# Performance work log

Hardware: AMD Instinct MI355X
Metric: run time of the kernel (lower is better)

## Reference

```python
import jax, jax.numpy as jnp
import numpy as np

B = 4096        # batch_size
D = 256         # feature_dim
N = 9000000     # dataset size (state buffer length)
G = 100         # num_groups
ALPHA = 0.5     # alpha_weight
GAMMA = 0.8
RHO = 8.0
LAM = 1.0       # lambada
ETA_P = 0.01
EPS = 1e-14
CLIP = 5.0


def setup_inputs() -> dict:
    key = jax.random.key(0)
    k = jax.random.split(key, 6)
    zis = jax.random.normal(k[0], (B, D), jnp.float32)
    zjs = jax.random.normal(k[1], (B, D), jnp.float32)
    # per-sample learned temperatures, small positive values
    taus_I = 0.01 + 0.2 * jax.random.uniform(k[2], (N,), jnp.float32)
    taus_T = 0.01 + 0.2 * jax.random.uniform(k[3], (N,), jnp.float32)
    group_info_I = jax.random.randint(k[4], (N,), 0, G, dtype=jnp.int32)
    group_info_T = jax.random.randint(k[5], (N,), 0, G, dtype=jnp.int32)
    ids = jnp.arange(B, dtype=jnp.int32)  # unique sample indices
    zeros_N = jnp.zeros((N,), jnp.float32)
    return {
        "zis": zis, "zjs": zjs,
        "s_I": zeros_N, "s_T": zeros_N, "b_I": zeros_N, "b_T": zeros_N,
        "z_I": jnp.zeros((G,), jnp.float32), "z_T": jnp.zeros((G,), jnp.float32),
        "p_I": jnp.ones((G,), jnp.float32) / G, "p_T": jnp.ones((G,), jnp.float32) / G,
        "taus_I": taus_I, "taus_T": taus_T,
        "ids": ids, "group_info_I": group_info_I, "group_info_T": group_info_T,
    }


def _l2norm(x):
    return x / jnp.maximum(jnp.linalg.norm(x, axis=1, keepdims=True), 1e-12)


def reference(zis, zjs, s_I, s_T, b_I, b_T, z_I, z_T, p_I, p_T,
              taus_I, taus_T, ids, group_info_I, group_info_T):
    zis = _l2norm(zis)
    zjs = _l2norm(zjs)
    sim = zis @ zjs.T                                   # [B, B]
    diag = jnp.diagonal(sim)                            # [B]
    mask_neg = 1.0 - jnp.eye(B, dtype=sim.dtype)
    image_diffs = sim - diag[:, None]
    text_diffs = sim - diag[None, :]

    tau_I = taus_I[ids]                                 # [B]
    tau_T = taus_T[ids]
    idt = jax.lax.stop_gradient(image_diffs / tau_I[:, None])
    tdt = jax.lax.stop_gradient(text_diffs / tau_T[None, :])

    # running max state (numerically-stable exp)
    old_b_I = b_I[ids]
    b_I_new = jnp.maximum(jnp.max(idt, axis=1), old_b_I)    # [B]
    old_b_T = b_T[ids]
    b_T_new = jnp.maximum(jnp.max(tdt, axis=0), old_b_T)    # [B]
    b_I = b_I.at[ids].set(b_I_new)
    b_T = b_T.at[ids].set(b_T_new)

    exp_I = jnp.exp(idt - b_I_new[:, None]) * mask_neg
    exp_T = jnp.exp(tdt - b_T_new[None, :]) * mask_neg
    g_I = jnp.sum(exp_I, axis=1)                         # [B]
    g_T = jnp.sum(exp_T, axis=0)                         # [B]

    # EMA of softmax denominators with max-rescaling
    s_I_new = (1.0 - GAMMA) * s_I[ids] * jnp.exp(old_b_I - b_I_new) + GAMMA * g_I
    s_T_new = (1.0 - GAMMA) * s_T[ids] * jnp.exp(old_b_T - b_T_new) + GAMMA * g_T
    s_I = s_I.at[ids].set(s_I_new)
    s_T = s_T.at[ids].set(s_T_new)
    s_I_c = jnp.maximum(s_I_new, EPS)
    s_T_c = jnp.maximum(s_T_new, EPS)

    w_I = exp_I / s_I_c[:, None]
    w_T = exp_T / s_T_c[None, :]

    gid_I = group_info_I[ids]                            # [B]
    gid_T = group_info_T[ids]
    gw_I = G * p_I[gid_I]                                # [B]
    gw_T = G * p_T[gid_T]

    image_loss = jnp.sum(w_I * gw_I[:, None] * image_diffs, axis=1)   # [B]
    text_loss = jnp.sum(w_T * gw_T[None, :] * text_diffs, axis=0)     # [B]
    total_loss = ALPHA * image_loss.mean() + (1.0 - ALPHA) * text_loss.mean()

    # per-group adversarial weight update
    F_I = tau_I * (jnp.log(s_I_c) + b_I_new + RHO)       # [B]
    F_T = tau_T * (jnp.log(s_T_c) + b_T_new + RHO)
    ones_b = jnp.ones((B,), sim.dtype)
    cnt_I = jnp.maximum(jax.ops.segment_sum(ones_b, gid_I, num_segments=G), 1.0)
    cnt_T = jnp.maximum(jax.ops.segment_sum(ones_b, gid_T, num_segments=G), 1.0)
    grad_p_I = jax.ops.segment_sum(F_I, gid_I, num_segments=G) / cnt_I
    grad_p_T = jax.ops.segment_sum(F_T, gid_T, num_segments=G) / cnt_T

    z_I = (1.0 - GAMMA) * z_I + GAMMA * grad_p_I
    z_T = (1.0 - GAMMA) * z_T + GAMMA * grad_p_T
    grad_hp_I = -LAM * jnp.log(p_I + EPS) - LAM
    grad_hp_T = -LAM * jnp.log(p_T + EPS) - LAM
    new_p_I = p_I * jnp.exp(2.0 * ETA_P * jnp.clip(z_I + grad_hp_I, -CLIP, CLIP))
    new_p_T = p_T * jnp.exp(2.0 * ETA_P * jnp.clip(z_T + grad_hp_T, -CLIP, CLIP))
    p_I = new_p_I / new_p_I.sum()
    p_T = new_p_T / new_p_T.sum()

    return total_loss, p_I, p_T
```

## Files before the change

### kernel.cpp

```cpp
#include <hip/hip_runtime.h>
#include <hip/hip_bf16.h>
#include <math.h>

#define BB 4096
#define DD 256
#define GG 100
#define GAMMA_C 0.8f
#define RHO_C 8.0f
#define ALPHA_C 0.5f
#define EPS_C 1e-14f
#define NS2 64

typedef __bf16 bf16x8 __attribute__((ext_vector_type(8)));
typedef float f32x4 __attribute__((ext_vector_type(4)));

__device__ inline int swz(int r, int k) {
    return ((r >> 4) << 12) | ((k >> 5) << 9) | (((k >> 3) & 3) << 7) |
           ((r & 15) << 3) | (k & 7);
}

__device__ inline float blockReduceSum(float v, float* lds) {
    for (int o = 32; o > 0; o >>= 1) v += __shfl_down(v, o);
    int lane = threadIdx.x & 63, wid = threadIdx.x >> 6;
    if (lane == 0) lds[wid] = v;
    __syncthreads();
    if (threadIdx.x == 0) {
        float r = lds[0];
        int nw = blockDim.x >> 6;
        for (int w = 1; w < nw; w++) r += lds[w];
        lds[0] = r;
    }
    __syncthreads();
    float r = lds[0];
    __syncthreads();
    return r;
}

__global__ void norm_kernel(const float* __restrict__ zis,
                            const float* __restrict__ zjs,
                            ushort* __restrict__ zhi, ushort* __restrict__ zlo,
                            ushort* __restrict__ whi, ushort* __restrict__ wlo,
                            float* __restrict__ diag, float* __restrict__ acc) {
    __shared__ float lds[8];
    int r = blockIdx.x;
    if (r == 0) { acc[threadIdx.x] = 0.f; acc[threadIdx.x + 256] = 0.f; }
    float zv = zis[r * DD + threadIdx.x];
    float wv = zjs[r * DD + threadIdx.x];
    float sz = blockReduceSum(zv * zv, lds);
    float sw = blockReduceSum(wv * wv, lds);
    float nz = zv * (1.0f / fmaxf(sqrtf(sz), 1e-12f));
    float nw = wv * (1.0f / fmaxf(sqrtf(sw), 1e-12f));
    float dt = blockReduceSum(nz * nw, lds);
    if (threadIdx.x == 0) diag[r] = dt;
    __hip_bfloat16 hz = __float2bfloat16(nz);
    __hip_bfloat16 lz = __float2bfloat16(nz - __bfloat162float(hz));
    __hip_bfloat16 hw = __float2bfloat16(nw);
    __hip_bfloat16 lw = __float2bfloat16(nw - __bfloat162float(hw));
    int si = swz(r, threadIdx.x);
    zhi[si] = *(ushort*)&hz;
    zlo[si] = *(ushort*)&lz;
    whi[si] = *(ushort*)&hw;
    wlo[si] = *(ushort*)&lw;
}

__global__ void __launch_bounds__(256, 4) fused_tile(const ushort* __restrict__ Ahi,
        const ushort* __restrict__ Alo, const ushort* __restrict__ Bhi,
        const ushort* __restrict__ Blo, const float* __restrict__ diag,
        const float* __restrict__ tausI, const float* __restrict__ tausT,
        const int* __restrict__ ids,
        float* __restrict__ pmR, float* __restrict__ pgR, float* __restrict__ pwR,
        float* __restrict__ pmC, float* __restrict__ pgC, float* __restrict__ pwC) {
    __shared__ float rDiag[128], rITau[128];
    __shared__ float cDiag[128], cITau[128];

    int lane = threadIdx.x & 63;
    int wv = threadIdx.x >> 6;
    int wm = wv >> 1, wn = wv & 1;
    int bm = blockIdx.y * 128, bn = blockIdx.x * 128;
    int ml = lane & 15, kq = lane >> 4;

    if (threadIdx.x < 128) {
        int r = bm + threadIdx.x;
        rDiag[threadIdx.x] = diag[r];
        rITau[threadIdx.x] = 1.0f / tausI[ids[r]];
    } else {
        int c = bn + threadIdx.x - 128;
        cDiag[threadIdx.x - 128] = diag[c];
        cITau[threadIdx.x - 128] = 1.0f / tausT[ids[c]];
    }

    int aBlk = (bm >> 4) + wm * 4;
    int bBlk = (bn >> 4) + wn * 4;
    int lofs = lane * 8;

    f32x4 acc[4][4] = {};
#pragma unroll
    for (int s = 0; s < 8; s++) {
        int so = s * 512 + lofs;
        bf16x8 ah[4], al[4], bh[4], bl[4];
#pragma unroll
        for (int t = 0; t < 4; t++) {
            ah[t] = *(const bf16x8*)&Ahi[(aBlk + t) * 4096 + so];
            al[t] = *(const bf16x8*)&Alo[(aBlk + t) * 4096 + so];
            bh[t] = *(const bf16x8*)&Bhi[(bBlk + t) * 4096 + so];
            bl[t] = *(const bf16x8*)&Blo[(bBlk + t) * 4096 + so];
        }
#pragma unroll
        for (int t = 0; t < 4; t++)
#pragma unroll
            for (int u = 0; u < 4; u++) {
                acc[t][u] = __builtin_amdgcn_mfma_f32_16x16x32_bf16(ah[t], bh[u], acc[t][u], 0, 0, 0);
                acc[t][u] = __builtin_amdgcn_mfma_f32_16x16x32_bf16(ah[t], bl[u], acc[t][u], 0, 0, 0);
                acc[t][u] = __builtin_amdgcn_mfma_f32_16x16x32_bf16(al[t], bh[u], acc[t][u], 0, 0, 0);
            }
    }
    __syncthreads();

    float rd[4][4], rit[4][4];
    for (int t = 0; t < 4; t++)
        for (int reg = 0; reg < 4; reg++) {
            int rl = wm * 64 + t * 16 + kq * 4 + reg;
            rd[t][reg] = rDiag[rl];
            rit[t][reg] = rITau[rl];
        }
    float blocR[4][4];
    for (int t = 0; t < 4; t++)
        for (int reg = 0; reg < 4; reg++) {
            float m = fmaxf(fmaxf(acc[t][0][reg], acc[t][1][reg]),
                            fmaxf(acc[t][2][reg], acc[t][3][reg]));
            for (int mask = 1; mask <= 8; mask <<= 1)
                m = fmaxf(m, __shfl_xor(m, mask));
            blocR[t][reg] = (m - rd[t][reg]) * rit[t][reg];
        }
    float cd[4], cit[4], cbloc[4];
    for (int u = 0; u < 4; u++) {
        int cl = wn * 64 + u * 16 + ml;
        cd[u] = cDiag[cl];
        cit[u] = cITau[cl];
        float m = -INFINITY;
        for (int t = 0; t < 4; t++)
            for (int reg = 0; reg < 4; reg++)
                m = fmaxf(m, acc[t][u][reg]);
        for (int mask = 16; mask <= 32; mask <<= 1)
            m = fmaxf(m, __shfl_xor(m, mask));
        cbloc[u] = (m - cd[u]) * cit[u];
    }
    float rg[4][4] = {}, rw[4][4] = {}, cg[4] = {}, cw[4] = {};
    for (int t = 0; t < 4; t++) {
        int gr0 = bm + wm * 64 + t * 16 + kq * 4;
        for (int u = 0; u < 4; u++) {
            int gc = bn + wn * 64 + u * 16 + ml;
            for (int reg = 0; reg < 4; reg++) {
                float v = acc[t][u][reg];
                bool off = (gr0 + reg) != gc;
                float dvI = v - rd[t][reg];
                float eI = off ? __expf(dvI * rit[t][reg] - blocR[t][reg]) : 0.f;
                rg[t][reg] += eI;
                rw[t][reg] += eI * dvI;
                float dvT = v - cd[u];
                float eT = off ? __expf(dvT * cit[u] - cbloc[u]) : 0.f;
                cg[u] += eT;
                cw[u] += eT * dvT;
            }
        }
    }
    int stripeR = blockIdx.x * 2 + wn;
    for (int t = 0; t < 4; t++) {
        for (int reg = 0; reg < 4; reg++)
            for (int mask = 1; mask <= 8; mask <<= 1) {
                rg[t][reg] += __shfl_xor(rg[t][reg], mask);
                rw[t][reg] += __shfl_xor(rw[t][reg], mask);
            }
        if (ml == 0) {
            size_t o = (size_t)stripeR * BB + bm + wm * 64 + t * 16 + kq * 4;
            *(float4*)&pmR[o] = make_float4(blocR[t][0], blocR[t][1], blocR[t][2], blocR[t][3]);
            *(float4*)&pgR[o] = make_float4(rg[t][0], rg[t][1], rg[t][2], rg[t][3]);
            *(float4*)&pwR[o] = make_float4(rw[t][0], rw[t][1], rw[t][2], rw[t][3]);
        }
    }
    int stripeC = blockIdx.y * 2 + wm;
    for (int u = 0; u < 4; u++) {
        for (int mask = 16; mask <= 32; mask <<= 1) {
            cg[u] += __shfl_xor(cg[u], mask);
            cw[u] += __shfl_xor(cw[u], mask);
        }
        if (kq == 0) {
            size_t o = (size_t)stripeC * BB + bn + wn * 64 + u * 16 + ml;
            pmC[o] = cbloc[u];
            pgC[o] = cg[u];
            pwC[o] = cw[u];
        }
    }
}

__global__ void __launch_bounds__(256) fin_kernel(
        const float* __restrict__ pmR, const float* __restrict__ pgR,
        const float* __restrict__ pwR, const float* __restrict__ pmC,
        const float* __restrict__ pgC, const float* __restrict__ pwC,
        const float* __restrict__ sI, const float* __restrict__ bI,
        const float* __restrict__ tausI, const int* __restrict__ gInfI,
        const float* __restrict__ pI,
        const float* __restrict__ sT, const float* __restrict__ bT,
        const float* __restrict__ tausT, const int* __restrict__ gInfT,
        const float* __restrict__ pT,
        const int* __restrict__ ids, float* __restrict__ acc,
        const float* __restrict__ zI, const float* __restrict__ zT,
        float* __restrict__ out) {
    __shared__ float lds[8];
    __shared__ float binF[GG], binC[GG];
    __shared__ int lastFlag;
    if (threadIdx.x < GG) { binF[threadIdx.x] = 0.f; binC[threadIdx.x] = 0.f; }
    __syncthreads();
    int side = blockIdx.x >> 4;
    int i = (blockIdx.x & 15) * 256 + threadIdx.x;
    const float* pm = side ? pmC : pmR;
    const float* pg = side ? pgC : pgR;
    const float* pw = side ? pwC : pwR;
    const float* sS = side ? sT : sI;
    const float* bS = side ? bT : bI;
    const float* taus = side ? tausT : tausI;
    const int* ginfo = side ? gInfT : gInfI;
    const float* pP = side ? pT : pI;

    int id = ids[i];
    float oldb = bS[id];
    float m = -INFINITY;
    for (int s = 0; s < NS2; s++) m = fmaxf(m, pm[(size_t)s * BB + i]);
    float bfin = fmaxf(m, oldb);
    float g = 0.f, wsum = 0.f;
    for (int s = 0; s < NS2; s++) {
        float f = __expf(pm[(size_t)s * BB + i] - bfin);
        g += pg[(size_t)s * BB + i] * f;
        wsum += pw[(size_t)s * BB + i] * f;
    }
    float tau = taus[id];
    float snew = (1.f - GAMMA_C) * sS[id] * expf(oldb - bfin) + GAMMA_C * g;
    float sc = fmaxf(snew, EPS_C);
    int gid = ginfo[id];
    float gw = (float)GG * pP[gid];
    float loss = gw * wsum / sc;
    float F = tau * (logf(sc) + bfin + RHO_C);
    atomicAdd(&binF[gid], F);
    atomicAdd(&binC[gid], 1.0f);
    float lsum = blockReduceSum(loss, lds);
    if (threadIdx.x == 0) atomicAdd(&acc[side], lsum);
    __syncthreads();
    if (threadIdx.x < GG) {
        atomicAdd(&acc[2 + side * 200 + threadIdx.x], binF[threadIdx.x]);
        atomicAdd(&acc[102 + side * 200 + threadIdx.x], binC[threadIdx.x]);
    }

    __threadfence();
    if (threadIdx.x == 0) {
        int old = atomicAdd((int*)&acc[408], 1);
        lastFlag = (old == 31);
    }
    __syncthreads();
    if (!lastFlag) return;

    int gg = threadIdx.x;
    float npI = 0.f, npT = 0.f;
    if (gg < GG) {
        float cI = __hip_atomic_load(&acc[102 + gg], __ATOMIC_RELAXED, __HIP_MEMORY_SCOPE_AGENT);
        float fI = __hip_atomic_load(&acc[2 + gg], __ATOMIC_RELAXED, __HIP_MEMORY_SCOPE_AGENT);
        float gpI = fI / fmaxf(cI, 1.f);
        float zi = (1.f - GAMMA_C) * zI[gg] + GAMMA_C * gpI;
        float ghpI = -logf(pI[gg] + EPS_C) - 1.f;
        float ti = fminf(fmaxf(zi + ghpI, -5.f), 5.f);
        npI = pI[gg] * expf(0.02f * ti);

        float cT = __hip_atomic_load(&acc[302 + gg], __ATOMIC_RELAXED, __HIP_MEMORY_SCOPE_AGENT);
        float fT = __hip_atomic_load(&acc[202 + gg], __ATOMIC_RELAXED, __HIP_MEMORY_SCOPE_AGENT);
        float gpT = fT / fmaxf(cT, 1.f);
        float zt = (1.f - GAMMA_C) * zT[gg] + GAMMA_C * gpT;
        float ghpT = -logf(pT[gg] + EPS_C) - 1.f;
        float tt = fminf(fmaxf(zt + ghpT, -5.f), 5.f);
        npT = pT[gg] * expf(0.02f * tt);
    }
    float sumI = blockReduceSum(npI, lds);
    float sumT = blockReduceSum(npT, lds);
    if (gg < GG) {
        out[1 + gg] = npI / sumI;
        out[101 + gg] = npT / sumT;
    }
    if (gg == 0) {
        float lI = __hip_atomic_load(&acc[0], __ATOMIC_RELAXED, __HIP_MEMORY_SCOPE_AGENT);
        float lT = __hip_atomic_load(&acc[1], __ATOMIC_RELAXED, __HIP_MEMORY_SCOPE_AGENT);
        out[0] = ALPHA_C * (lI / (float)BB) + (1.f - ALPHA_C) * (lT / (float)BB);
    }
}

extern "C" void kernel_launch(void* const* d_in, const int* in_sizes, int n_in,
                              void* d_out, int out_size, void* d_ws, size_t ws_size,
                              hipStream_t stream) {
    const float* zis   = (const float*)d_in[0];
    const float* zjs   = (const float*)d_in[1];
    const float* s_I   = (const float*)d_in[2];
    const float* s_T   = (const float*)d_in[3];
    const float* b_I   = (const float*)d_in[4];
    const float* b_T   = (const float*)d_in[5];
    const float* z_I   = (const float*)d_in[6];
    const float* z_T   = (const float*)d_in[7];
    const float* p_I   = (const float*)d_in[8];
    const float* p_T   = (const float*)d_in[9];
    const float* tausI = (const float*)d_in[10];
    const float* tausT = (const float*)d_in[11];
    const int*   ids   = (const int*)d_in[12];
    const int*   gInfI = (const int*)d_in[13];
    const int*   gInfT = (const int*)d_in[14];
    float* out = (float*)d_out;

    char* ws = (char*)d_ws;
    ushort* zhi = (ushort*)ws;
    ushort* zlo = zhi + (size_t)BB * DD;
    ushort* whi = zlo + (size_t)BB * DD;
    ushort* wlo = whi + (size_t)BB * DD;
    float* acc  = (float*)(wlo + (size_t)BB * DD);
    float* diag = acc + 512;
    float* pmR  = diag + BB;
    float* pgR  = pmR + (size_t)NS2 * BB;
    float* pwR  = pgR + (size_t)NS2 * BB;
    float* pmC  = pwR + (size_t)NS2 * BB;
    float* pgC  = pmC + (size_t)NS2 * BB;
    float* pwC  = pgC + (size_t)NS2 * BB;

    norm_kernel<<<BB, 256, 0, stream>>>(zis, zjs, zhi, zlo, whi, wlo, diag, acc);
    fused_tile<<<dim3(32, 32), 256, 0, stream>>>(zhi, zlo, whi, wlo, diag,
            tausI, tausT, ids, pmR, pgR, pwR, pmC, pgC, pwC);
    fin_kernel<<<32, 256, 0, stream>>>(pmR, pgR, pwR, pmC, pgC, pwC,
            s_I, b_I, tausI, gInfI, p_I, s_T, b_T, tausT, gInfT, p_T, ids, acc,
            z_I, z_T, out);
}
```

Measured before the change: 321.4 us.

## Switch similarity GEMM to 32x32x16 MFMA with matching operand swizzle

Replaces the 16x16x32 bf16 MFMA tiling with 32x32x16 MFMA instructions, changing the bf16 split-operand swizzle layout to match the 32-row operand blocks. The epilogue is reorganised to fit the new accumulator lane mapping, and the row-wise softmax reductions are processed in groups of four rows so fewer registers are live at once. The aim is fewer instructions and operand loads per tile and lower register pressure. The price is a longer shuffle reduction chain across 32 lanes for the row statistics.

```diff
diff --git a/kernel.cpp b/kernel.cpp
--- a/kernel.cpp
+++ b/kernel.cpp
@@ -12,11 +12,11 @@
 #define NS2 64
 
 typedef __bf16 bf16x8 __attribute__((ext_vector_type(8)));
-typedef float f32x4 __attribute__((ext_vector_type(4)));
-
-__device__ inline int swz(int r, int k) {
-    return ((r >> 4) << 12) | ((k >> 5) << 9) | (((k >> 3) & 3) << 7) |
-           ((r & 15) << 3) | (k & 7);
+typedef float f32x16 __attribute__((ext_vector_type(16)));
+
+__device__ inline int swz32(int r, int k) {
+    return ((r >> 5) << 13) | ((k >> 4) << 9) |
+           (((((k >> 3) & 1) << 5) | (r & 31)) << 3) | (k & 7);
 }
 
 __device__ inline float blockReduceSum(float v, float* lds) {
@@ -56,7 +56,7 @@
     __hip_bfloat16 lz = __float2bfloat16(nz - __bfloat162float(hz));
     __hip_bfloat16 hw = __float2bfloat16(nw);
     __hip_bfloat16 lw = __float2bfloat16(nw - __bfloat162float(hw));
-    int si = swz(r, threadIdx.x);
+    int si = swz32(r, threadIdx.x);
     zhi[si] = *(ushort*)&hz;
     zlo[si] = *(ushort*)&lz;
     whi[si] = *(ushort*)&hw;
@@ -77,7 +77,7 @@
     int wv = threadIdx.x >> 6;
     int wm = wv >> 1, wn = wv & 1;
     int bm = blockIdx.y * 128, bn = blockIdx.x * 128;
-    int ml = lane & 15, kq = lane >> 4;
+    int h = lane >> 5, cl = lane & 31;
 
     if (threadIdx.x < 128) {
         int r = bm + threadIdx.x;
@@ -89,108 +89,113 @@
         cITau[threadIdx.x - 128] = 1.0f / tausT[ids[c]];
     }
 
-    int aBlk = (bm >> 4) + wm * 4;
-    int bBlk = (bn >> 4) + wn * 4;
+    int aBlk = (bm >> 5) + wm * 2;
+    int bBlk = (bn >> 5) + wn * 2;
     int lofs = lane * 8;
 
-    f32x4 acc[4][4] = {};
+    f32x16 acc[2][2] = {};
 #pragma unroll
-    for (int s = 0; s < 8; s++) {
+    for (int s = 0; s < 16; s++) {
         int so = s * 512 + lofs;
-        bf16x8 ah[4], al[4], bh[4], bl[4];
+        bf16x8 ah[2], al[2], bh[2], bl[2];
 #pragma unroll
-        for (int t = 0; t < 4; t++) {
-            ah[t] = *(const bf16x8*)&Ahi[(aBlk + t) * 4096 + so];
-            al[t] = *(const bf16x8*)&Alo[(aBlk + t) * 4096 + so];
-            bh[t] = *(const bf16x8*)&Bhi[(bBlk + t) * 4096 + so];
-            bl[t] = *(const bf16x8*)&Blo[(bBlk + t) * 4096 + so];
+        for (int t = 0; t < 2; t++) {
+            ah[t] = *(const bf16x8*)&Ahi[(aBlk + t) * 8192 + so];
+            al[t] = *(const bf16x8*)&Alo[(aBlk + t) * 8192 + so];
+            bh[t] = *(const bf16x8*)&Bhi[(bBlk + t) * 8192 + so];
+            bl[t] = *(const bf16x8*)&Blo[(bBlk + t) * 8192 + so];
         }
 #pragma unroll
-        for (int t = 0; t < 4; t++)
+        for (int t = 0; t < 2; t++)
 #pragma unroll
-            for (int u = 0; u < 4; u++) {
-                acc[t][u] = __builtin_amdgcn_mfma_f32_16x16x32_bf16(ah[t], bh[u], acc[t][u], 0, 0, 0);
-                acc[t][u] = __builtin_amdgcn_mfma_f32_16x16x32_bf16(ah[t], bl[u], acc[t][u], 0, 0, 0);
-                acc[t][u] = __builtin_amdgcn_mfma_f32_16x16x32_bf16(al[t], bh[u], acc[t][u], 0, 0, 0);
-            }
-    }
-    __syncthreads();
-
-    float rd[4][4], rit[4][4];
-    for (int t = 0; t < 4; t++)
-        for (int reg = 0; reg < 4; reg++) {
-            int rl = wm * 64 + t * 16 + kq * 4 + reg;
-            rd[t][reg] = rDiag[rl];
-            rit[t][reg] = rITau[rl];
-        }
-    float blocR[4][4];
-    for (int t = 0; t < 4; t++)
-        for (int reg = 0; reg < 4; reg++) {
-            float m = fmaxf(fmaxf(acc[t][0][reg], acc[t][1][reg]),
-                            fmaxf(acc[t][2][reg], acc[t][3][reg]));
-            for (int mask = 1; mask <= 8; mask <<= 1)
-                m = fmaxf(m, __shfl_xor(m, mask));
-            blocR[t][reg] = (m - rd[t][reg]) * rit[t][reg];
-        }
-    float cd[4], cit[4], cbloc[4];
-    for (int u = 0; u < 4; u++) {
-        int cl = wn * 64 + u * 16 + ml;
-        cd[u] = cDiag[cl];
-        cit[u] = cITau[cl];
+            for (int u = 0; u < 2; u++) {
+                acc[t][u] = __builtin_amdgcn_mfma_f32_32x32x16_bf16(ah[t], bh[u], acc[t][u], 0, 0, 0);
+                acc[t][u] = __builtin_amdgcn_mfma_f32_32x32x16_bf16(ah[t], bl[u], acc[t][u], 0, 0, 0);
+                acc[t][u] = __builtin_amdgcn_mfma_f32_32x32x16_bf16(al[t], bh[u], acc[t][u], 0, 0, 0);
+            }
+    }
+    __syncthreads();
+
+    float cd[2], cit[2];
+    for (int u = 0; u < 2; u++) {
+        int clloc = wn * 64 + u * 32 + cl;
+        cd[u] = cDiag[clloc];
+        cit[u] = cITau[clloc];
+    }
+
+    float cbloc[2], cg[2] = {}, cw[2] = {};
+    for (int u = 0; u < 2; u++) {
         float m = -INFINITY;
-        for (int t = 0; t < 4; t++)
-            for (int reg = 0; reg < 4; reg++)
+        for (int t = 0; t < 2; t++)
+            for (int reg = 0; reg < 16; reg++)
                 m = fmaxf(m, acc[t][u][reg]);
-        for (int mask = 16; mask <= 32; mask <<= 1)
-            m = fmaxf(m, __shfl_xor(m, mask));
+        m = fmaxf(m, __shfl_xor(m, 32));
         cbloc[u] = (m - cd[u]) * cit[u];
     }
-    float rg[4][4] = {}, rw[4][4] = {}, cg[4] = {}, cw[4] = {};
-    for (int t = 0; t < 4; t++) {
-        int gr0 = bm + wm * 64 + t * 16 + kq * 4;
-        for (int u = 0; u < 4; u++) {
-            int gc = bn + wn * 64 + u * 16 + ml;
-            for (int reg = 0; reg < 4; reg++) {
+    for (int t = 0; t < 2; t++)
+        for (int u = 0; u < 2; u++) {
+            int gc = bn + wn * 64 + u * 32 + cl;
+            for (int reg = 0; reg < 16; reg++) {
+                int gr = bm + wm * 64 + t * 32 + (reg & 3) + 4 * h + 8 * (reg >> 2);
                 float v = acc[t][u][reg];
-                bool off = (gr0 + reg) != gc;
-                float dvI = v - rd[t][reg];
-                float eI = off ? __expf(dvI * rit[t][reg] - blocR[t][reg]) : 0.f;
-                rg[t][reg] += eI;
-                rw[t][reg] += eI * dvI;
+                bool off = gr != gc;
                 float dvT = v - cd[u];
                 float eT = off ? __expf(dvT * cit[u] - cbloc[u]) : 0.f;
                 cg[u] += eT;
                 cw[u] += eT * dvT;
             }
         }
-    }
-    int stripeR = blockIdx.x * 2 + wn;
-    for (int t = 0; t < 4; t++) {
-        for (int reg = 0; reg < 4; reg++)
-            for (int mask = 1; mask <= 8; mask <<= 1) {
-                rg[t][reg] += __shfl_xor(rg[t][reg], mask);
-                rw[t][reg] += __shfl_xor(rw[t][reg], mask);
-            }
-        if (ml == 0) {
-            size_t o = (size_t)stripeR * BB + bm + wm * 64 + t * 16 + kq * 4;
-            *(float4*)&pmR[o] = make_float4(blocR[t][0], blocR[t][1], blocR[t][2], blocR[t][3]);
-            *(float4*)&pgR[o] = make_float4(rg[t][0], rg[t][1], rg[t][2], rg[t][3]);
-            *(float4*)&pwR[o] = make_float4(rw[t][0], rw[t][1], rw[t][2], rw[t][3]);
-        }
-    }
     int stripeC = blockIdx.y * 2 + wm;
-    for (int u = 0; u < 4; u++) {
-        for (int mask = 16; mask <= 32; mask <<= 1) {
-            cg[u] += __shfl_xor(cg[u], mask);
-            cw[u] += __shfl_xor(cw[u], mask);
-        }
-        if (kq == 0) {
-            size_t o = (size_t)stripeC * BB + bn + wn * 64 + u * 16 + ml;
+    for (int u = 0; u < 2; u++) {
+        cg[u] += __shfl_xor(cg[u], 32);
+        cw[u] += __shfl_xor(cw[u], 32);
+        if (h == 0) {
+            size_t o = (size_t)stripeC * BB + bn + wn * 64 + u * 32 + cl;
             pmC[o] = cbloc[u];
             pgC[o] = cg[u];
             pwC[o] = cw[u];
         }
     }
+
+    int stripeR = blockIdx.x * 2 + wn;
+    for (int t = 0; t < 2; t++)
+        for (int q = 0; q < 4; q++) {
+            float rd4[4], rit4[4], bloc[4], rg[4] = {}, rw[4] = {};
+            for (int j = 0; j < 4; j++) {
+                int rl = wm * 64 + t * 32 + 8 * q + 4 * h + j;
+                rd4[j] = rDiag[rl];
+                rit4[j] = rITau[rl];
+            }
+            for (int j = 0; j < 4; j++) {
+                float m = fmaxf(acc[t][0][4 * q + j], acc[t][1][4 * q + j]);
+                for (int mask = 1; mask <= 16; mask <<= 1)
+                    m = fmaxf(m, __shfl_xor(m, mask));
+                bloc[j] = (m - rd4[j]) * rit4[j];
+            }
+            for (int u = 0; u < 2; u++) {
+                int gc = bn + wn * 64 + u * 32 + cl;
+                for (int j = 0; j < 4; j++) {
+                    int gr = bm + wm * 64 + t * 32 + 8 * q + 4 * h + j;
+                    float v = acc[t][u][4 * q + j];
+                    bool off = gr != gc;
+                    float dvI = v - rd4[j];
+                    float eI = off ? __expf(dvI * rit4[j] - bloc[j]) : 0.f;
+                    rg[j] += eI;
+                    rw[j] += eI * dvI;
+                }
+            }
+            for (int j = 0; j < 4; j++)
+                for (int mask = 1; mask <= 16; mask <<= 1) {
+                    rg[j] += __shfl_xor(rg[j], mask);
+                    rw[j] += __shfl_xor(rw[j], mask);
+                }
+            if (cl == 0) {
+                size_t o = (size_t)stripeR * BB + bm + wm * 64 + t * 32 + 8 * q + 4 * h;
+                *(float4*)&pmR[o] = make_float4(bloc[0], bloc[1], bloc[2], bloc[3]);
+                *(float4*)&pgR[o] = make_float4(rg[0], rg[1], rg[2], rg[3]);
+                *(float4*)&pwR[o] = make_float4(rw[0], rw[1], rw[2], rw[3]);
+            }
+        }
 }
 
 __global__ void __launch_bounds__(256) fin_kernel(
```

New measurement: 309.8 us. 1.04x faster.
